# Optimization experiments

Hardware: AMD Instinct MI355X
Metric: run time of the kernel (lower is better)

Reference implementation:

```python
import jax, jax.numpy as jnp
import numpy as np

EPS = 1e-5  # BatchNorm2d default eps


def _bn_params(c, gamma):
    # rows: gamma, beta, running_mean, running_var (inference-mode BN)
    return jnp.stack([jnp.full((c,), gamma, jnp.float32),
                      jnp.zeros((c,), jnp.float32),
                      jnp.zeros((c,), jnp.float32),
                      jnp.ones((c,), jnp.float32)])


def _bn(x, p):
    g, b, m, v = p
    scale = (g / jnp.sqrt(v + EPS)).reshape(1, -1, 1, 1)
    return (x - m.reshape(1, -1, 1, 1)) * scale + b.reshape(1, -1, 1, 1)


def _conv1x1(x, w, b):
    # w: [O, C]; 1x1 Conv2d == channel matmul
    return jnp.einsum('oc,nctv->notv', w, x) + b[None, :, None, None]


def setup_inputs() -> dict:
    key = jax.random.key(0)
    N, C, COUT, T, V, S = 8, 64, 128, 256, 256, 3
    IC = COUT // 4  # coff_embedding = 4
    ks = jax.random.split(key, 10)
    rn = lambda k, shp, s=0.05: jax.random.normal(k, shp, jnp.float32) * s
    x = jax.random.normal(ks[0], (N, C, T, V), jnp.float32)
    mat_adj = jax.random.uniform(ks[1], (S, T, T), jnp.float32) * (1.0 / T)  # static adjacency
    adj_weight = jnp.full((S, T, T), 1e-6, jnp.float32)  # nn.init.constant_(weight, 1e-6)
    return {
        'x': x,
        'mat_adj': mat_adj,
        'adj_weight': adj_weight,
        'wa': rn(ks[2], (S, IC, C)), 'ba': jnp.zeros((S, IC), jnp.float32),
        'wb': rn(ks[3], (S, IC, C)), 'bb': jnp.zeros((S, IC), jnp.float32),
        'wd': rn(ks[4], (S, COUT, C)), 'bd': jnp.zeros((S, COUT), jnp.float32),
        'gcn_bn': _bn_params(COUT, 1e-6),  # util.init_bn(self.bn, 1e-6)
        'cres_w': rn(ks[5], (COUT, C)), 'cres_b': jnp.zeros((COUT,), jnp.float32),
        'cres_bn': _bn_params(COUT, 1.0),
        'tcn_w': rn(ks[6], (COUT, COUT, 9)), 'tcn_b': jnp.zeros((COUT,), jnp.float32),
        'tcn_bn': _bn_params(COUT, 1.0),
        'rt_w': rn(ks[7], (COUT, C)), 'rt_b': jnp.zeros((COUT,), jnp.float32),
        'rt_bn': _bn_params(COUT, 1.0),
    }


def reference(x, mat_adj, adj_weight, wa, ba, wb, bb, wd, bd, gcn_bn,
              cres_w, cres_b, cres_bn, tcn_w, tcn_b, tcn_bn, rt_w, rt_b, rt_bn):
    N, C, T, V = x.shape
    A = mat_adj + adj_weight  # [S, T, T]
    y = 0.0
    for i in range(A.shape[0]):  # num_subset = 3, structurally distinct weights
        a = _conv1x1(x, wa[i], ba[i])      # [N, IC, T, V]
        be = _conv1x1(x, wb[i], bb[i])     # [N, IC, T, V]
        # embed1 [N,T,IC*V] @ embed2 [N,IC*V,T] -> contract over (IC, V)
        scores = jnp.einsum('nctv,ncsv->nts', a, be) / V
        att = jax.nn.softmax(scores, axis=-2)  # Softmax(dim=-2)
        adapt = A[i] + att                      # [N, T, T]
        # mat_inpt [N,C*V,T] @ adapt -> view(N,C,V,T)
        xa = jnp.einsum('nctv,nts->ncvs', x, adapt)  # [N, C, V, T]
        y = y + _conv1x1(xa, wd[i], bd[i])           # [N, COUT, V, T]
    gcn = jax.nn.relu(_bn(y, gcn_bn) + _bn(_conv1x1(x, cres_w, cres_b), cres_bn))
    # UnitTSCN: Conv2d kernel (9,1), stride (1,1), padding (4,0), then BN
    t = jax.lax.conv_general_dilated(gcn, tcn_w[..., None], (1, 1), ((4, 4), (0, 0)),
                                     dimension_numbers=('NCHW', 'OIHW', 'NCHW'))
    t = _bn(t + tcn_b[None, :, None, None], tcn_bn)
    # residual path: UnitTSCN(kernel_size=1, stride=1) since in != out
    r = _bn(_conv1x1(x, rt_w, rt_b), rt_bn)
    return jax.nn.relu(t + r)
```

## Files before the change

kernel.cpp:

```cpp
#include <hip/hip_runtime.h>

typedef unsigned short u16;

#define DEVI static __device__ __forceinline__

DEVI float bf2f(u16 v) { return __uint_as_float(((unsigned)v) << 16); }
DEVI u16 f2bf(float f) {
  unsigned u = __float_as_uint(f);
  u += 0x7FFFu + ((u >> 16) & 1u);
  return (u16)(u >> 16);
}
DEVI float4 ld4bf(const u16* p) {
  ushort4 q = *(const ushort4*)p;
  return make_float4(bf2f(q.x), bf2f(q.y), bf2f(q.z), bf2f(q.w));
}

typedef __attribute__((ext_vector_type(8))) short short8;
typedef __attribute__((ext_vector_type(4))) float floatx4;


__global__ void k_diag(float* out, float v) { out[0] = v; }

__global__ __launch_bounds__(256) void k_ab2(
    const float* __restrict__ x, const float* __restrict__ wa, const float* __restrict__ ba,
    const float* __restrict__ wb, const float* __restrict__ bb,
    u16* __restrict__ a_buf, u16* __restrict__ b_buf, int sub)
{
  __shared__ __align__(16) u16 Aw[64 * 64];
  __shared__ __align__(16) u16 Bx[256 * 64];
  __shared__ float sbias[64];
  const int n = blockIdx.y;
  const int q0 = blockIdx.x << 8;
  const int tid = threadIdx.x;

  if (tid < 64) {
    sbias[tid] = (tid < 32) ? ba[sub * 32 + tid] : bb[sub * 32 + tid - 32];
  }
  {
    const int kq = tid & 15;
    const int rr = tid >> 4;
    #pragma unroll
    for (int j = 0; j < 4; ++j) {
      int r = rr + (j << 4);
      float4 wv = (r < 32) ? *(const float4*)(wa + sub * 2048 + r * 64 + kq * 4)
                           : *(const float4*)(wb + sub * 2048 + (r - 32) * 64 + kq * 4);
      int e = (r << 6) + (((kq >> 1) ^ (r & 7)) << 3) + ((kq & 1) << 2);
      *(ushort4*)&Aw[e] = make_ushort4(f2bf(wv.x), f2bf(wv.y), f2bf(wv.z), f2bf(wv.w));
    }
  }
  {
    const int q4 = (tid & 63) << 2;
    const int kb = (tid >> 6) << 4;
    u16 va[16][4];
    #pragma unroll
    for (int dk = 0; dk < 16; ++dk) {
      float4 f = *(const float4*)(x + (((size_t)(n << 6) + kb + dk) << 16) + q0 + q4);
      va[dk][0] = f2bf(f.x); va[dk][1] = f2bf(f.y);
      va[dk][2] = f2bf(f.z); va[dk][3] = f2bf(f.w);
    }
    const int g0 = kb >> 3;
    #pragma unroll
    for (int dq = 0; dq < 4; ++dq) {
      int q = q4 + dq;
      int e0 = (q << 6) + ((g0 ^ (q & 7)) << 3);
      *(ushort4*)&Bx[e0]     = make_ushort4(va[0][dq], va[1][dq], va[2][dq], va[3][dq]);
      *(ushort4*)&Bx[e0 + 4] = make_ushort4(va[4][dq], va[5][dq], va[6][dq], va[7][dq]);
      int e1 = (q << 6) + (((g0 + 1) ^ (q & 7)) << 3);
      *(ushort4*)&Bx[e1]     = make_ushort4(va[8][dq], va[9][dq], va[10][dq], va[11][dq]);
      *(ushort4*)&Bx[e1 + 4] = make_ushort4(va[12][dq], va[13][dq], va[14][dq], va[15][dq]);
    }
  }
  __syncthreads();

  const int lane = tid & 63, wave = tid >> 6;
  const int qw = wave << 6;
  const int l15 = lane & 15, lg = lane >> 4;
  floatx4 acc[4][4];
  #pragma unroll
  for (int m = 0; m < 4; ++m)
    #pragma unroll
    for (int nn = 0; nn < 4; ++nn) acc[m][nn] = (floatx4){0.f, 0.f, 0.f, 0.f};

  #pragma unroll
  for (int ks = 0; ks < 2; ++ks) {
    const int gk = (ks << 2) + lg;
    short8 av[4], bv[4];
    #pragma unroll
    for (int m = 0; m < 4; ++m) {
      int r = (m << 4) + l15;
      av[m] = *(const short8*)&Aw[(r << 6) + ((gk ^ (r & 7)) << 3)];
    }
    #pragma unroll
    for (int nn = 0; nn < 4; ++nn) {
      int q = qw + (nn << 4) + l15;
      bv[nn] = *(const short8*)&Bx[(q << 6) + ((gk ^ (q & 7)) << 3)];
    }
    #pragma unroll
    for (int m = 0; m < 4; ++m)
      #pragma unroll
      for (int nn = 0; nn < 4; ++nn)
        acc[m][nn] = __builtin_amdgcn_mfma_f32_16x16x32_bf16(av[m], bv[nn], acc[m][nn], 0, 0, 0);
  }

  #pragma unroll
  for (int m = 0; m < 4; ++m) {
    #pragma unroll
    for (int r = 0; r < 4; ++r) {
      int row = (m << 4) + (lg << 2) + r;
      float bias = sbias[row];
      u16* dst = (row < 32) ? a_buf + (((n * 32 + row) << 16) + q0)
                            : b_buf + (((n * 32 + row - 32) << 16) + q0);
      #pragma unroll
      for (int nn = 0; nn < 4; ++nn) {
        int q = qw + (nn << 4) + l15;
        dst[q] = f2bf(acc[m][nn][r] + bias);
      }
    }
  }
}

__global__ __launch_bounds__(256) void k_sc2(
    const u16* __restrict__ a_buf, const u16* __restrict__ b_buf,
    float* __restrict__ part)
{
  __shared__ __align__(16) u16 At[128 * 64];
  __shared__ __align__(16) u16 Bt[128 * 64];
  const int n = blockIdx.z;
  const int kg = blockIdx.y;
  const int t0 = (blockIdx.x >> 1) << 7;
  const int s0 = (blockIdx.x & 1) << 7;
  const int tid = threadIdx.x;
  const int lane = tid & 63, wave = tid >> 6;
  const int tw = (wave & 1) << 6;
  const int sw = (wave >> 1) << 6;
  const int l15 = lane & 15, lg = lane >> 4;
  const int g = tid & 7;
  const int trow = tid >> 3;

  floatx4 acc[4][4];
  #pragma unroll
  for (int m = 0; m < 4; ++m)
    #pragma unroll
    for (int nn = 0; nn < 4; ++nn) acc[m][nn] = (floatx4){0.f, 0.f, 0.f, 0.f};

  for (int cc = 0; cc < 4; ++cc) {
    const int c = (kg << 2) + cc;
    const u16* ap = a_buf + ((n * 32 + c) << 16);
    const u16* bp = b_buf + ((n * 32 + c) << 16);
    for (int vt = 0; vt < 4; ++vt) {
      const int v0 = vt << 6;
      __syncthreads();
      #pragma unroll
      for (int j = 0; j < 4; ++j) {
        int t = trow + (j << 5);
        int e = (t << 6) + ((g ^ (t & 7)) << 3);
        *(short8*)&At[e] = *(const short8*)(ap + (t0 + t) * 256 + v0 + g * 8);
        *(short8*)&Bt[e] = *(const short8*)(bp + (s0 + t) * 256 + v0 + g * 8);
      }
      __syncthreads();
      #pragma unroll
      for (int ks = 0; ks < 2; ++ks) {
        const int gk = (ks << 2) + lg;
        short8 av[4], bv[4];
        #pragma unroll
        for (int m = 0; m < 4; ++m) {
          int t = tw + (m << 4) + l15;
          av[m] = *(const short8*)&At[(t << 6) + ((gk ^ (t & 7)) << 3)];
        }
        #pragma unroll
        for (int nn = 0; nn < 4; ++nn) {
          int s = sw + (nn << 4) + l15;
          bv[nn] = *(const short8*)&Bt[(s << 6) + ((gk ^ (s & 7)) << 3)];
        }
        #pragma unroll
        for (int m = 0; m < 4; ++m)
          #pragma unroll
          for (int nn = 0; nn < 4; ++nn)
            acc[m][nn] = __builtin_amdgcn_mfma_f32_16x16x32_bf16(av[m], bv[nn], acc[m][nn], 0, 0, 0);
      }
    }
  }

  const float inv256 = 1.0f / 256.0f;
  float* pp = part + (((kg << 3) + n) << 16);
  #pragma unroll
  for (int m = 0; m < 4; ++m) {
    #pragma unroll
    for (int r = 0; r < 4; ++r) {
      int t = t0 + tw + (m << 4) + (lg << 2) + r;
      #pragma unroll
      for (int nn = 0; nn < 4; ++nn) {
        int s = s0 + sw + (nn << 4) + l15;
        pp[t * 256 + s] = acc[m][nn][r] * inv256;
      }
    }
  }
}

__global__ __launch_bounds__(256) void k_soft2(
    const float* __restrict__ part, const float* __restrict__ madj,
    const float* __restrict__ wadj, float* __restrict__ adapt, int sub)
{
  __shared__ float Ls[256][32];
  __shared__ float redm[8][32];
  __shared__ float reds[8][32];
  const int sc = blockIdx.x;
  const int n = blockIdx.y;
  const int tid = threadIdx.x;
  const int sl = tid & 31, tg = tid >> 5;
  const int s = (sc << 5) + sl;

  float m = -1e30f;
  for (int i = 0; i < 32; ++i) {
    int t = (tg << 5) + i;
    int off = t * 256 + s;
    float v = 0.f;
    #pragma unroll
    for (int k = 0; k < 8; ++k) v += part[(((k << 3) + n) << 16) + off];
    Ls[t][sl] = v;
    m = fmaxf(m, v);
  }
  redm[tg][sl] = m;
  __syncthreads();
  #pragma unroll
  for (int k = 0; k < 8; ++k) m = fmaxf(m, redm[k][sl]);
  float sum = 0.f;
  for (int i = 0; i < 32; ++i) {
    int t = (tg << 5) + i;
    sum += __expf(Ls[t][sl] - m);
  }
  reds[tg][sl] = sum;
  __syncthreads();
  float tot = 0.f;
  #pragma unroll
  for (int k = 0; k < 8; ++k) tot += reds[k][sl];
  float inv = 1.0f / tot;
  const float* ma = madj + (sub << 16);
  const float* wa2 = wadj + (sub << 16);
  float* adp = adapt + (n << 16);
  for (int i = 0; i < 32; ++i) {
    int t = (tg << 5) + i;
    int off = t * 256 + s;
    adp[off] = __expf(Ls[t][sl] - m) * inv + ma[off] + wa2[off];
  }
}

__global__ __launch_bounds__(256) void k_xa2(
    const float* __restrict__ x, const float* __restrict__ adapt,
    u16* __restrict__ xa)
{
  __shared__ __align__(16) u16 Av[128 * 64];
  __shared__ __align__(16) u16 Bs2[128 * 64];
  const int n = blockIdx.z, c = blockIdx.y;
  const int v0 = (blockIdx.x >> 1) << 7;
  const int s0 = (blockIdx.x & 1) << 7;
  const int tid = threadIdx.x;
  const int lane = tid & 63, wave = tid >> 6;
  const int vw = (wave & 1) << 6;
  const int sw = (wave >> 1) << 6;
  const int l15 = lane & 15, lg = lane >> 4;
  const int q4 = (tid & 31) << 2;
  const int kb = (tid >> 5) << 3;
  const float* xp = x + (((size_t)(n << 6) + c) << 16);
  const float* ap = adapt + (n << 16);

  floatx4 acc[4][4];
  #pragma unroll
  for (int m = 0; m < 4; ++m)
    #pragma unroll
    for (int nn = 0; nn < 4; ++nn) acc[m][nn] = (floatx4){0.f, 0.f, 0.f, 0.f};

  for (int kt = 0; kt < 4; ++kt) {
    const int tb = kt << 6;
    __syncthreads();
    {
      u16 va[8][4], vb[8][4];
      #pragma unroll
      for (int dk = 0; dk < 8; ++dk) {
        int t = tb + kb + dk;
        float4 fa = *(const float4*)(xp + (t << 8) + v0 + q4);
        float4 fb = *(const float4*)(ap + (t << 8) + s0 + q4);
        va[dk][0] = f2bf(fa.x); va[dk][1] = f2bf(fa.y);
        va[dk][2] = f2bf(fa.z); va[dk][3] = f2bf(fa.w);
        vb[dk][0] = f2bf(fb.x); vb[dk][1] = f2bf(fb.y);
        vb[dk][2] = f2bf(fb.z); vb[dk][3] = f2bf(fb.w);
      }
      const int g = kb >> 3;
      #pragma unroll
      for (int dq = 0; dq < 4; ++dq) {
        int q = q4 + dq;
        int e = (q << 6) + ((g ^ (q & 7)) << 3);
        *(ushort4*)&Av[e]      = make_ushort4(va[0][dq], va[1][dq], va[2][dq], va[3][dq]);
        *(ushort4*)&Av[e + 4]  = make_ushort4(va[4][dq], va[5][dq], va[6][dq], va[7][dq]);
        *(ushort4*)&Bs2[e]     = make_ushort4(vb[0][dq], vb[1][dq], vb[2][dq], vb[3][dq]);
        *(ushort4*)&Bs2[e + 4] = make_ushort4(vb[4][dq], vb[5][dq], vb[6][dq], vb[7][dq]);
      }
    }
    __syncthreads();
    #pragma unroll
    for (int ks = 0; ks < 2; ++ks) {
      const int gk = (ks << 2) + lg;
      short8 av[4], bv[4];
      #pragma unroll
      for (int m = 0; m < 4; ++m) {
        int v = vw + (m << 4) + l15;
        av[m] = *(const short8*)&Av[(v << 6) + ((gk ^ (v & 7)) << 3)];
      }
      #pragma unroll
      for (int nn = 0; nn < 4; ++nn) {
        int s = sw + (nn << 4) + l15;
        bv[nn] = *(const short8*)&Bs2[(s << 6) + ((gk ^ (s & 7)) << 3)];
      }
      #pragma unroll
      for (int m = 0; m < 4; ++m)
        #pragma unroll
        for (int nn = 0; nn < 4; ++nn)
          acc[m][nn] = __builtin_amdgcn_mfma_f32_16x16x32_bf16(av[m], bv[nn], acc[m][nn], 0, 0, 0);
    }
  }

  u16* xo = xa + (((n << 6) + c) << 16);
  #pragma unroll
  for (int m = 0; m < 4; ++m) {
    #pragma unroll
    for (int r = 0; r < 4; ++r) {
      int v = v0 + vw + (m << 4) + (lg << 2) + r;
      #pragma unroll
      for (int nn = 0; nn < 4; ++nn) {
        int s = s0 + sw + (nn << 4) + l15;
        xo[v * 256 + s] = f2bf(acc[m][nn][r]);
      }
    }
  }
}

__global__ __launch_bounds__(256) void k_gcnf(
    const u16* __restrict__ xa_all, const float* __restrict__ x,
    const float* __restrict__ wd, const float* __restrict__ bd,
    const float* __restrict__ cw, const float* __restrict__ cb,
    const float* __restrict__ cbn, const float* __restrict__ gbn,
    u16* __restrict__ gcn)
{
  __shared__ __align__(16) u16 Wt[128 * 64];
  __shared__ __align__(16) u16 Gt[128 * 64];
  __shared__ float s_kk[128], s_sg[128], s_sc[128];
  const int n = blockIdx.y;
  const int q0 = blockIdx.x << 7;
  const int tid = threadIdx.x;
  if (tid < 128) {
    int o = tid;
    float sg = gbn[o] * rsqrtf(gbn[384 + o] + 1e-5f);
    float sc = cbn[o] * rsqrtf(cbn[384 + o] + 1e-5f);
    s_sg[o] = sg; s_sc[o] = sc;
    s_kk[o] = sg * (bd[o] + bd[128 + o] + bd[256 + o])
            + (cb[o] - cbn[256 + o]) * sc + cbn[128 + o]
            - gbn[256 + o] * sg + gbn[128 + o];
  }
  __syncthreads();

  const int lane = tid & 63, wave = tid >> 6;
  const int ow = (wave & 1) << 6;
  const int qw = (wave >> 1) << 6;
  const int l15 = lane & 15, lg = lane >> 4;
  const int kq = tid & 15;
  const int orow = tid >> 4;
  const int q4 = (tid & 31) << 2;
  const int kb = (tid >> 5) << 3;

  floatx4 acc[4][4];
  #pragma unroll
  for (int m = 0; m < 4; ++m)
    #pragma unroll
    for (int nn = 0; nn < 4; ++nn) acc[m][nn] = (floatx4){0.f, 0.f, 0.f, 0.f};

  for (int kt = 0; kt < 6; ++kt) {
    __syncthreads();
    #pragma unroll
    for (int j = 0; j < 8; ++j) {
      int o = orow + (j << 4);
      int e = (o << 6) + (((kq >> 1) ^ (o & 7)) << 3) + ((kq & 1) << 2);
      if (kt < 3) {
        float4 wv = *(const float4*)(wd + kt * 8192 + o * 64 + kq * 4);
        float s = s_sg[o];
        *(ushort4*)&Wt[e] = make_ushort4(f2bf(s * wv.x), f2bf(s * wv.y),
                                         f2bf(s * wv.z), f2bf(s * wv.w));
      } else {
        float4 wv = *(const float4*)(cw + o * 64 + kq * 4);
        float s = s_sc[o];
        float f0 = s * wv.x, f1 = s * wv.y, f2 = s * wv.z, f3 = s * wv.w;
        u16 h0 = f2bf(f0), h1 = f2bf(f1), h2 = f2bf(f2), h3 = f2bf(f3);
        if (kt == 4)
          *(ushort4*)&Wt[e] = make_ushort4(f2bf(f0 - bf2f(h0)), f2bf(f1 - bf2f(h1)),
                                           f2bf(f2 - bf2f(h2)), f2bf(f3 - bf2f(h3)));
        else
          *(ushort4*)&Wt[e] = make_ushort4(h0, h1, h2, h3);
      }
    }
    {
      u16 va[8][4];
      if (kt < 3) {
        const u16* xp = xa_all + (size_t)kt * 33554432u + (((size_t)(n << 6) + kb) << 16);
        #pragma unroll
        for (int dk = 0; dk < 8; ++dk) {
          ushort4 t4 = *(const ushort4*)(xp + ((size_t)dk << 16) + q0 + q4);
          va[dk][0] = t4.x; va[dk][1] = t4.y; va[dk][2] = t4.z; va[dk][3] = t4.w;
        }
      } else {
        #pragma unroll
        for (int dk = 0; dk < 8; ++dk) {
          float4 f = *(const float4*)(x + (((size_t)(n << 6) + kb + dk) << 16) + q0 + q4);
          if (kt == 5) {
            u16 h0 = f2bf(f.x), h1 = f2bf(f.y), h2 = f2bf(f.z), h3 = f2bf(f.w);
            va[dk][0] = f2bf(f.x - bf2f(h0)); va[dk][1] = f2bf(f.y - bf2f(h1));
            va[dk][2] = f2bf(f.z - bf2f(h2)); va[dk][3] = f2bf(f.w - bf2f(h3));
          } else {
            va[dk][0] = f2bf(f.x); va[dk][1] = f2bf(f.y);
            va[dk][2] = f2bf(f.z); va[dk][3] = f2bf(f.w);
          }
        }
      }
      const int g = kb >> 3;
      #pragma unroll
      for (int dq = 0; dq < 4; ++dq) {
        int q = q4 + dq;
        int e = (q << 6) + ((g ^ (q & 7)) << 3);
        *(ushort4*)&Gt[e]     = make_ushort4(va[0][dq], va[1][dq], va[2][dq], va[3][dq]);
        *(ushort4*)&Gt[e + 4] = make_ushort4(va[4][dq], va[5][dq], va[6][dq], va[7][dq]);
      }
    }
    __syncthreads();
    #pragma unroll
    for (int ks = 0; ks < 2; ++ks) {
      const int gk = (ks << 2) + lg;
      short8 av[4], bv[4];
      #pragma unroll
      for (int m = 0; m < 4; ++m) {
        int o = ow + (m << 4) + l15;
        av[m] = *(const short8*)&Wt[(o << 6) + ((gk ^ (o & 7)) << 3)];
      }
      #pragma unroll
      for (int nn = 0; nn < 4; ++nn) {
        int q = qw + (nn << 4) + l15;
        bv[nn] = *(const short8*)&Gt[(q << 6) + ((gk ^ (q & 7)) << 3)];
      }
      #pragma unroll
      for (int m = 0; m < 4; ++m)
        #pragma unroll
        for (int nn = 0; nn < 4; ++nn)
          acc[m][nn] = __builtin_amdgcn_mfma_f32_16x16x32_bf16(av[m], bv[nn], acc[m][nn], 0, 0, 0);
    }
  }

  #pragma unroll
  for (int m = 0; m < 4; ++m) {
    #pragma unroll
    for (int r = 0; r < 4; ++r) {
      int o = ow + (m << 4) + (lg << 2) + r;
      float kadd = s_kk[o];
      u16* dst = gcn + (((n << 7) + o) << 16) + q0;
      #pragma unroll
      for (int nn = 0; nn < 4; ++nn) {
        int q = qw + (nn << 4) + l15;
        dst[q] = f2bf(fmaxf(acc[m][nn][r] + kadd, 0.f));
      }
    }
  }
}

__global__ __launch_bounds__(256) void k_out(
    const u16* __restrict__ gcn, const float* __restrict__ x,
    const float* __restrict__ tw, const float* __restrict__ tb, const float* __restrict__ tbn,
    const float* __restrict__ rw, const float* __restrict__ rb, const float* __restrict__ rbn,
    float* __restrict__ out)
{
  __shared__ __align__(16) u16 Wh[128 * 64];
  __shared__ __align__(16) u16 Wl[128 * 64];
  __shared__ __align__(16) u16 Gc[128 * 64];
  __shared__ float s_st[128], s_sr[128], s_kk[128];
  const int n = blockIdx.y;
  const int q0 = blockIdx.x << 7;
  const int h = q0 >> 8;
  const int w0 = q0 & 255;
  const int tid = threadIdx.x;
  if (tid < 128) {
    int o = tid;
    float st = tbn[o] * rsqrtf(tbn[384 + o] + 1e-5f);
    float sr = rbn[o] * rsqrtf(rbn[384 + o] + 1e-5f);
    s_st[o] = st; s_sr[o] = sr;
    s_kk[o] = (tb[o] - tbn[256 + o]) * st + tbn[128 + o]
            + (rb[o] - rbn[256 + o]) * sr + rbn[128 + o];
  }
  __syncthreads();

  const int lane = tid & 63;
  const int wave = tid >> 6;
  const int ow = (wave & 1) << 6;
  const int qw = (wave >> 1) << 6;
  const int l15 = lane & 15;
  const int lg  = lane >> 4;

  const int kq   = tid & 15;
  const int orow = tid >> 4;
  const int q4   = (tid & 31) << 2;
  const int kb   = (tid >> 5) << 3;

  floatx4 acc[4][4];
  #pragma unroll
  for (int m = 0; m < 4; ++m)
    #pragma unroll
    for (int nn = 0; nn < 4; ++nn)
      acc[m][nn] = (floatx4){0.f, 0.f, 0.f, 0.f};

  for (int kc = 0; kc < 19; ++kc) {
    __syncthreads();
    {
      const int k4 = (kc << 6) + (kq << 2);
      #pragma unroll
      for (int j = 0; j < 8; ++j) {
        int o = orow + (j << 4);
        float4 wv;
        float s;
        if (kc < 18) { wv = *(const float4*)(tw + o * 1152 + k4); s = s_st[o]; }
        else         { wv = *(const float4*)(rw + (o << 6) + (k4 - 1152)); s = s_sr[o]; }
        float f0 = s * wv.x, f1 = s * wv.y, f2 = s * wv.z, f3 = s * wv.w;
        u16 b0 = f2bf(f0), b1 = f2bf(f1), b2 = f2bf(f2), b3 = f2bf(f3);
        int e = (o << 6) + (((kq >> 1) ^ (o & 7)) << 3) + ((kq & 1) << 2);
        *(ushort4*)&Wh[e] = make_ushort4(b0, b1, b2, b3);
        *(ushort4*)&Wl[e] = make_ushort4(f2bf(f0 - bf2f(b0)), f2bf(f1 - bf2f(b1)),
                                         f2bf(f2 - bf2f(b2)), f2bf(f3 - bf2f(b3)));
      }
    }
    {
      u16 va[8][4];
      if (kc < 18) {
        #pragma unroll
        for (int dk = 0; dk < 8; ++dk) {
          int k = (kc << 6) + kb + dk;
          unsigned i = (unsigned)k / 9u;
          int kh = k - 9 * (int)i;
          int h2 = h + kh - 4;
          ushort4 t4;
          if ((unsigned)h2 < 256u)
            t4 = *(const ushort4*)(gcn + ((((n << 7) + (int)i) << 16) + (h2 << 8) + w0 + q4));
          else t4 = make_ushort4(0, 0, 0, 0);
          va[dk][0] = t4.x; va[dk][1] = t4.y; va[dk][2] = t4.z; va[dk][3] = t4.w;
        }
      } else {
        #pragma unroll
        for (int dk = 0; dk < 8; ++dk) {
          int c = kb + dk;
          float4 f = *(const float4*)(x + (((size_t)(n << 6) + c) << 16) + q0 + q4);
          va[dk][0] = f2bf(f.x); va[dk][1] = f2bf(f.y);
          va[dk][2] = f2bf(f.z); va[dk][3] = f2bf(f.w);
        }
      }
      #pragma unroll
      for (int dq = 0; dq < 4; ++dq) {
        int q = q4 + dq;
        int e = (q << 6) + ((((kb >> 3) ^ (q & 7))) << 3);
        *(ushort4*)&Gc[e]     = make_ushort4(va[0][dq], va[1][dq], va[2][dq], va[3][dq]);
        *(ushort4*)&Gc[e + 4] = make_ushort4(va[4][dq], va[5][dq], va[6][dq], va[7][dq]);
      }
    }
    __syncthreads();
    #pragma unroll
    for (int ks = 0; ks < 2; ++ks) {
      const int gk = (ks << 2) + lg;
      short8 ah[4], al[4], bg[4];
      #pragma unroll
      for (int m = 0; m < 4; ++m) {
        int o = ow + (m << 4) + l15;
        int e = (o << 6) + ((gk ^ (o & 7)) << 3);
        ah[m] = *(const short8*)&Wh[e];
        al[m] = *(const short8*)&Wl[e];
      }
      #pragma unroll
      for (int nn = 0; nn < 4; ++nn) {
        int q = qw + (nn << 4) + l15;
        int e = (q << 6) + ((gk ^ (q & 7)) << 3);
        bg[nn] = *(const short8*)&Gc[e];
      }
      #pragma unroll
      for (int m = 0; m < 4; ++m)
        #pragma unroll
        for (int nn = 0; nn < 4; ++nn) {
          acc[m][nn] = __builtin_amdgcn_mfma_f32_16x16x32_bf16(ah[m], bg[nn], acc[m][nn], 0, 0, 0);
          acc[m][nn] = __builtin_amdgcn_mfma_f32_16x16x32_bf16(al[m], bg[nn], acc[m][nn], 0, 0, 0);
        }
    }
  }

  #pragma unroll
  for (int m = 0; m < 4; ++m) {
    #pragma unroll
    for (int r = 0; r < 4; ++r) {
      int o = ow + (m << 4) + (lg << 2) + r;
      float kadd = s_kk[o];
      float* dst = out + (((size_t)((n << 7) + o)) << 16) + q0;
      #pragma unroll
      for (int nn = 0; nn < 4; ++nn) {
        int q = qw + (nn << 4) + l15;
        dst[q] = fmaxf(acc[m][nn][r] + kadd, 0.f);
      }
    }
  }
}

extern "C" void kernel_launch(void* const* d_in, const int* in_sizes, int n_in,
                              void* d_out, int out_size, void* d_ws, size_t ws_size,
                              hipStream_t stream) {
  const float* x       = (const float*)d_in[0];
  const float* mat_adj = (const float*)d_in[1];
  const float* adj_w   = (const float*)d_in[2];
  const float* wa      = (const float*)d_in[3];
  const float* ba      = (const float*)d_in[4];
  const float* wb      = (const float*)d_in[5];
  const float* bb      = (const float*)d_in[6];
  const float* wd      = (const float*)d_in[7];
  const float* bd      = (const float*)d_in[8];
  const float* gcn_bn  = (const float*)d_in[9];
  const float* cres_w  = (const float*)d_in[10];
  const float* cres_b  = (const float*)d_in[11];
  const float* cres_bn = (const float*)d_in[12];
  const float* tcn_w   = (const float*)d_in[13];
  const float* tcn_b   = (const float*)d_in[14];
  const float* tcn_bn  = (const float*)d_in[15];
  const float* rt_w    = (const float*)d_in[16];
  const float* rt_b    = (const float*)d_in[17];
  const float* rt_bn   = (const float*)d_in[18];
  float* out = (float*)d_out;

  (void)hipGetLastError();

  hipMemsetAsync(d_out, 0x42, 4, stream);

  if (n_in != 19)                    { k_diag<<<1,1,0,stream>>>(out, 2019.f); return; }
  if (in_sizes[0]  != 33554432)      { k_diag<<<1,1,0,stream>>>(out, 2000.f); return; }
  if (in_sizes[3]  != 6144)          { k_diag<<<1,1,0,stream>>>(out, 2003.f); return; }
  if (in_sizes[7]  != 24576)         { k_diag<<<1,1,0,stream>>>(out, 2007.f); return; }
  if (in_sizes[9]  != 512)           { k_diag<<<1,1,0,stream>>>(out, 2009.f); return; }
  if (in_sizes[13] != 147456)        { k_diag<<<1,1,0,stream>>>(out, 2013.f); return; }
  if (in_sizes[16] != 8192)          { k_diag<<<1,1,0,stream>>>(out, 2016.f); return; }
  if (out_size != 67108864)          { k_diag<<<1,1,0,stream>>>(out, 3000.f); return; }
  if (ws_size < 134217728ull)        { k_diag<<<1,1,0,stream>>>(out, (float)ws_size); return; }

  float* wsf   = (float*)d_ws;
  u16*   a_buf = (u16*)d_ws;
  u16*   b_buf = a_buf + 16777216;
  float* part  = wsf + 16777216;
  float* adapt = wsf + 20971520;
  u16*   gcn   = (u16*)d_ws;
  u16*   xa_all = (u16*)d_out;

  for (int i = 0; i < 3; ++i) {
    k_ab2  <<<dim3(256, 8),   256, 0, stream>>>(x, wa, ba, wb, bb, a_buf, b_buf, i);
    k_sc2  <<<dim3(4, 8, 8),  256, 0, stream>>>(a_buf, b_buf, part);
    k_soft2<<<dim3(8, 8),     256, 0, stream>>>(part, mat_adj, adj_w, adapt, i);
    k_xa2  <<<dim3(4, 64, 8), 256, 0, stream>>>(x, adapt, xa_all + (size_t)i * 33554432u);
  }
  k_gcnf<<<dim3(512, 8), 256, 0, stream>>>(xa_all, x, wd, bd, cres_w, cres_b,
                                           cres_bn, gcn_bn, gcn);
  k_out<<<dim3(512, 8), 256, 0, stream>>>(gcn, x, tcn_w, tcn_b, tcn_bn,
                                          rt_w, rt_b, rt_bn, out);

  hipError_t le = hipGetLastError();
  if (le != hipSuccess) {
    k_diag<<<1, 1, 0, stream>>>(out, 1.0e9f + (float)(int)le);
  }
}
```

Baseline: 1.502 ms.

## Pre-transpose x to bf16 once, use packed bf16 converts and new LDS swizzle

Adds a k_xt kernel that converts x to bf16 and transposes it to [N,C,V,T] once. The three k_xa2 launches then load their A operand as direct 16-byte bf16 copies instead of reconverting fp32 x with scattered 4-element LDS stores each time. Every fp32->bf16 conversion now uses the packed v_cvt_pk_bf16_f32 instruction. LDS staging stores are widened to 16-byte writes with a two-level XOR swizzle, and per-lane LDS offsets are precomputed outside the k-loops. The cost is an extra launch and an extra bf16 copy of x stored in the spare tail of the output buffer.

```diff
diff --git a/kernel.cpp b/kernel.cpp
--- a/kernel.cpp
+++ b/kernel.cpp
@@ -10,16 +10,56 @@
   u += 0x7FFFu + ((u >> 16) & 1u);
   return (u16)(u >> 16);
 }
-DEVI float4 ld4bf(const u16* p) {
-  ushort4 q = *(const ushort4*)p;
-  return make_float4(bf2f(q.x), bf2f(q.y), bf2f(q.z), bf2f(q.w));
+DEVI unsigned pk2bf(float a, float b) {
+  unsigned r;
+  asm("v_cvt_pk_bf16_f32 %0, %1, %2" : "=v"(r) : "v"(a), "v"(b));
+  return r;
 }
 
 typedef __attribute__((ext_vector_type(8))) short short8;
 typedef __attribute__((ext_vector_type(4))) float floatx4;
 
+#define GSWZ(q, g) (((q) << 6) + ((((g) ^ ((q) & 7) ^ (((q) >> 3) & 7))) << 3))
+
 
 __global__ void k_diag(float* out, float v) { out[0] = v; }
+
+__global__ __launch_bounds__(256) void k_xt(
+    const float* __restrict__ x, u16* __restrict__ xt)
+{
+  __shared__ __align__(16) u16 Ls[256 * 64];
+  const int n = blockIdx.z, c = blockIdx.y, t0 = blockIdx.x << 6;
+  const int tid = threadIdx.x;
+  const float* xp = x + (((size_t)(n << 6) + c) << 16);
+  const int t4 = (tid & 15) << 2;
+  #pragma unroll
+  for (int j = 0; j < 4; ++j) {
+    const int v4 = ((tid >> 4) << 2) + (j << 6);
+    float4 f0 = *(const float4*)(xp + ((t0 + t4 + 0) << 8) + v4);
+    float4 f1 = *(const float4*)(xp + ((t0 + t4 + 1) << 8) + v4);
+    float4 f2 = *(const float4*)(xp + ((t0 + t4 + 2) << 8) + v4);
+    float4 f3 = *(const float4*)(xp + ((t0 + t4 + 3) << 8) + v4);
+    const float fr[4][4] = {{f0.x,f1.x,f2.x,f3.x},{f0.y,f1.y,f2.y,f3.y},
+                            {f0.z,f1.z,f2.z,f3.z},{f0.w,f1.w,f2.w,f3.w}};
+    #pragma unroll
+    for (int dv = 0; dv < 4; ++dv) {
+      int v = v4 + dv;
+      unsigned p0 = pk2bf(fr[dv][0], fr[dv][1]);
+      unsigned p1 = pk2bf(fr[dv][2], fr[dv][3]);
+      int e = (v << 6) + (((t4 >> 3) ^ (v & 7)) << 3) + (t4 & 4);
+      *(uint2*)&Ls[e] = make_uint2(p0, p1);
+    }
+  }
+  __syncthreads();
+  const int g = tid & 7;
+  u16* xo = xt + (((size_t)((n << 6) + c)) << 16) + t0;
+  #pragma unroll
+  for (int it = 0; it < 8; ++it) {
+    int v = (tid >> 3) + (it << 5);
+    short8 row = *(const short8*)&Ls[(v << 6) + ((g ^ (v & 7)) << 3)];
+    *(short8*)(xo + (v << 8) + (g << 3)) = row;
+  }
+}
 
 __global__ __launch_bounds__(256) void k_ab2(
     const float* __restrict__ x, const float* __restrict__ wa, const float* __restrict__ ba,
@@ -33,41 +73,37 @@
   const int q0 = blockIdx.x << 8;
   const int tid = threadIdx.x;
 
-  if (tid < 64) {
-    sbias[tid] = (tid < 32) ? ba[sub * 32 + tid] : bb[sub * 32 + tid - 32];
-  }
+  if (tid < 64) sbias[tid] = (tid < 32) ? ba[sub * 32 + tid] : bb[sub * 32 + tid - 32];
   {
     const int kq = tid & 15;
     const int rr = tid >> 4;
     #pragma unroll
     for (int j = 0; j < 4; ++j) {
       int r = rr + (j << 4);
-      float4 wv = (r < 32) ? *(const float4*)(wa + sub * 2048 + r * 64 + kq * 4)
-                           : *(const float4*)(wb + sub * 2048 + (r - 32) * 64 + kq * 4);
+      float4 wv = (r < 32) ? *(const float4*)(wa + sub * 2048 + r * 64 + (kq << 2))
+                           : *(const float4*)(wb + sub * 2048 + (r - 32) * 64 + (kq << 2));
       int e = (r << 6) + (((kq >> 1) ^ (r & 7)) << 3) + ((kq & 1) << 2);
-      *(ushort4*)&Aw[e] = make_ushort4(f2bf(wv.x), f2bf(wv.y), f2bf(wv.z), f2bf(wv.w));
+      *(uint2*)&Aw[e] = make_uint2(pk2bf(wv.x, wv.y), pk2bf(wv.z, wv.w));
     }
   }
   {
     const int q4 = (tid & 63) << 2;
     const int kb = (tid >> 6) << 4;
-    u16 va[16][4];
-    #pragma unroll
-    for (int dk = 0; dk < 16; ++dk) {
-      float4 f = *(const float4*)(x + (((size_t)(n << 6) + kb + dk) << 16) + q0 + q4);
-      va[dk][0] = f2bf(f.x); va[dk][1] = f2bf(f.y);
-      va[dk][2] = f2bf(f.z); va[dk][3] = f2bf(f.w);
-    }
-    const int g0 = kb >> 3;
-    #pragma unroll
-    for (int dq = 0; dq < 4; ++dq) {
-      int q = q4 + dq;
-      int e0 = (q << 6) + ((g0 ^ (q & 7)) << 3);
-      *(ushort4*)&Bx[e0]     = make_ushort4(va[0][dq], va[1][dq], va[2][dq], va[3][dq]);
-      *(ushort4*)&Bx[e0 + 4] = make_ushort4(va[4][dq], va[5][dq], va[6][dq], va[7][dq]);
-      int e1 = (q << 6) + (((g0 + 1) ^ (q & 7)) << 3);
-      *(ushort4*)&Bx[e1]     = make_ushort4(va[8][dq], va[9][dq], va[10][dq], va[11][dq]);
-      *(ushort4*)&Bx[e1 + 4] = make_ushort4(va[12][dq], va[13][dq], va[14][dq], va[15][dq]);
+    #pragma unroll
+    for (int half = 0; half < 2; ++half) {
+      float fa[8][4];
+      #pragma unroll
+      for (int dk = 0; dk < 8; ++dk)
+        *(float4*)fa[dk] = *(const float4*)(x + (((size_t)(n << 6) + kb + half * 8 + dk) << 16) + q0 + q4);
+      const int G = (kb >> 3) + half;
+      #pragma unroll
+      for (int dq = 0; dq < 4; ++dq) {
+        unsigned w0 = pk2bf(fa[0][dq], fa[1][dq]);
+        unsigned w1 = pk2bf(fa[2][dq], fa[3][dq]);
+        unsigned w2 = pk2bf(fa[4][dq], fa[5][dq]);
+        unsigned w3 = pk2bf(fa[6][dq], fa[7][dq]);
+        *(uint4*)&Bx[GSWZ(q4 + dq, G)] = make_uint4(w0, w1, w2, w3);
+      }
     }
   }
   __syncthreads();
@@ -75,6 +111,12 @@
   const int lane = tid & 63, wave = tid >> 6;
   const int qw = wave << 6;
   const int l15 = lane & 15, lg = lane >> 4;
+  int aoff[4], boff[4];
+  #pragma unroll
+  for (int m = 0; m < 4; ++m) { int r = (m << 4) + l15; aoff[m] = (r << 6) + ((r & 7) << 3); }
+  #pragma unroll
+  for (int nn = 0; nn < 4; ++nn) { int q = qw + (nn << 4) + l15; boff[nn] = GSWZ(q, 0); }
+
   floatx4 acc[4][4];
   #pragma unroll
   for (int m = 0; m < 4; ++m)
@@ -83,18 +125,12 @@
 
   #pragma unroll
   for (int ks = 0; ks < 2; ++ks) {
-    const int gk = (ks << 2) + lg;
+    const int gs = ((ks << 2) + lg) << 3;
     short8 av[4], bv[4];
     #pragma unroll
-    for (int m = 0; m < 4; ++m) {
-      int r = (m << 4) + l15;
-      av[m] = *(const short8*)&Aw[(r << 6) + ((gk ^ (r & 7)) << 3)];
-    }
-    #pragma unroll
-    for (int nn = 0; nn < 4; ++nn) {
-      int q = qw + (nn << 4) + l15;
-      bv[nn] = *(const short8*)&Bx[(q << 6) + ((gk ^ (q & 7)) << 3)];
-    }
+    for (int m = 0; m < 4; ++m) av[m] = *(const short8*)&Aw[aoff[m] ^ gs];
+    #pragma unroll
+    for (int nn = 0; nn < 4; ++nn) bv[nn] = *(const short8*)&Bx[boff[nn] ^ gs];
     #pragma unroll
     for (int m = 0; m < 4; ++m)
       #pragma unroll
@@ -111,9 +147,10 @@
       u16* dst = (row < 32) ? a_buf + (((n * 32 + row) << 16) + q0)
                             : b_buf + (((n * 32 + row - 32) << 16) + q0);
       #pragma unroll
-      for (int nn = 0; nn < 4; ++nn) {
-        int q = qw + (nn << 4) + l15;
-        dst[q] = f2bf(acc[m][nn][r] + bias);
+      for (int np = 0; np < 2; ++np) {
+        unsigned p = pk2bf(acc[m][2 * np][r] + bias, acc[m][2 * np + 1][r] + bias);
+        dst[qw + np * 32 + l15] = (u16)p;
+        dst[qw + np * 32 + 16 + l15] = (u16)(p >> 16);
       }
     }
   }
@@ -137,6 +174,12 @@
   const int g = tid & 7;
   const int trow = tid >> 3;
 
+  int aoff[4], boff[4];
+  #pragma unroll
+  for (int m = 0; m < 4; ++m) { int t = tw + (m << 4) + l15; aoff[m] = (t << 6) + ((t & 7) << 3); }
+  #pragma unroll
+  for (int nn = 0; nn < 4; ++nn) { int s = sw + (nn << 4) + l15; boff[nn] = (s << 6) + ((s & 7) << 3); }
+
   floatx4 acc[4][4];
   #pragma unroll
   for (int m = 0; m < 4; ++m)
@@ -160,18 +203,12 @@
       __syncthreads();
       #pragma unroll
       for (int ks = 0; ks < 2; ++ks) {
-        const int gk = (ks << 2) + lg;
+        const int gs = ((ks << 2) + lg) << 3;
         short8 av[4], bv[4];
         #pragma unroll
-        for (int m = 0; m < 4; ++m) {
-          int t = tw + (m << 4) + l15;
-          av[m] = *(const short8*)&At[(t << 6) + ((gk ^ (t & 7)) << 3)];
-        }
-        #pragma unroll
-        for (int nn = 0; nn < 4; ++nn) {
-          int s = sw + (nn << 4) + l15;
-          bv[nn] = *(const short8*)&Bt[(s << 6) + ((gk ^ (s & 7)) << 3)];
-        }
+        for (int m = 0; m < 4; ++m) av[m] = *(const short8*)&At[aoff[m] ^ gs];
+        #pragma unroll
+        for (int nn = 0; nn < 4; ++nn) bv[nn] = *(const short8*)&Bt[boff[nn] ^ gs];
         #pragma unroll
         for (int m = 0; m < 4; ++m)
           #pragma unroll
@@ -246,23 +283,28 @@
 }
 
 __global__ __launch_bounds__(256) void k_xa2(
-    const float* __restrict__ x, const float* __restrict__ adapt,
+    const u16* __restrict__ xt, const float* __restrict__ adapt,
     u16* __restrict__ xa)
 {
   __shared__ __align__(16) u16 Av[128 * 64];
-  __shared__ __align__(16) u16 Bs2[128 * 64];
+  __shared__ __align__(16) u16 Bt2[128 * 64];
   const int n = blockIdx.z, c = blockIdx.y;
   const int v0 = (blockIdx.x >> 1) << 7;
   const int s0 = (blockIdx.x & 1) << 7;
   const int tid = threadIdx.x;
   const int lane = tid & 63, wave = tid >> 6;
-  const int vw = (wave & 1) << 6;
-  const int sw = (wave >> 1) << 6;
+  const int vw = (wave & 1) << 6, sw = (wave >> 1) << 6;
   const int l15 = lane & 15, lg = lane >> 4;
-  const int q4 = (tid & 31) << 2;
-  const int kb = (tid >> 5) << 3;
-  const float* xp = x + (((size_t)(n << 6) + c) << 16);
+  const int ga = tid & 7, vr = tid >> 3;
+  const int q4 = (tid & 31) << 2, kb = (tid >> 5) << 3;
+  const u16* xp = xt + (((size_t)((n << 6) + c)) << 16);
   const float* ap = adapt + (n << 16);
+
+  int aoff[4], boff[4];
+  #pragma unroll
+  for (int m = 0; m < 4; ++m) { int v = vw + (m << 4) + l15; aoff[m] = (v << 6) + ((v & 7) << 3); }
+  #pragma unroll
+  for (int nn = 0; nn < 4; ++nn) { int s = sw + (nn << 4) + l15; boff[nn] = GSWZ(s, 0); }
 
   floatx4 acc[4][4];
   #pragma unroll
@@ -273,44 +315,36 @@
   for (int kt = 0; kt < 4; ++kt) {
     const int tb = kt << 6;
     __syncthreads();
+    #pragma unroll
+    for (int j = 0; j < 4; ++j) {
+      int v = vr + (j << 5);
+      *(short8*)&Av[(v << 6) + ((ga ^ (v & 7)) << 3)] =
+        *(const short8*)(xp + ((v0 + v) << 8) + tb + (ga << 3));
+    }
     {
-      u16 va[8][4], vb[8][4];
-      #pragma unroll
-      for (int dk = 0; dk < 8; ++dk) {
-        int t = tb + kb + dk;
-        float4 fa = *(const float4*)(xp + (t << 8) + v0 + q4);
-        float4 fb = *(const float4*)(ap + (t << 8) + s0 + q4);
-        va[dk][0] = f2bf(fa.x); va[dk][1] = f2bf(fa.y);
-        va[dk][2] = f2bf(fa.z); va[dk][3] = f2bf(fa.w);
-        vb[dk][0] = f2bf(fb.x); vb[dk][1] = f2bf(fb.y);
-        vb[dk][2] = f2bf(fb.z); vb[dk][3] = f2bf(fb.w);
-      }
-      const int g = kb >> 3;
+      float fa[8][4];
+      #pragma unroll
+      for (int dk = 0; dk < 8; ++dk)
+        *(float4*)fa[dk] = *(const float4*)(ap + ((tb + kb + dk) << 8) + s0 + q4);
+      const int G = kb >> 3;
       #pragma unroll
       for (int dq = 0; dq < 4; ++dq) {
-        int q = q4 + dq;
-        int e = (q << 6) + ((g ^ (q & 7)) << 3);
-        *(ushort4*)&Av[e]      = make_ushort4(va[0][dq], va[1][dq], va[2][dq], va[3][dq]);
-        *(ushort4*)&Av[e + 4]  = make_ushort4(va[4][dq], va[5][dq], va[6][dq], va[7][dq]);
-        *(ushort4*)&Bs2[e]     = make_ushort4(vb[0][dq], vb[1][dq], vb[2][dq], vb[3][dq]);
-        *(ushort4*)&Bs2[e + 4] = make_ushort4(vb[4][dq], vb[5][dq], vb[6][dq], vb[7][dq]);
+        unsigned w0 = pk2bf(fa[0][dq], fa[1][dq]);
+        unsigned w1 = pk2bf(fa[2][dq], fa[3][dq]);
+        unsigned w2 = pk2bf(fa[4][dq], fa[5][dq]);
+        unsigned w3 = pk2bf(fa[6][dq], fa[7][dq]);
+        *(uint4*)&Bt2[GSWZ(q4 + dq, G)] = make_uint4(w0, w1, w2, w3);
       }
     }
     __syncthreads();
     #pragma unroll
     for (int ks = 0; ks < 2; ++ks) {
-      const int gk = (ks << 2) + lg;
+      const int gs = ((ks << 2) + lg) << 3;
       short8 av[4], bv[4];
       #pragma unroll
-      for (int m = 0; m < 4; ++m) {
-        int v = vw + (m << 4) + l15;
-        av[m] = *(const short8*)&Av[(v << 6) + ((gk ^ (v & 7)) << 3)];
-      }
-      #pragma unroll
-      for (int nn = 0; nn < 4; ++nn) {
-        int s = sw + (nn << 4) + l15;
-        bv[nn] = *(const short8*)&Bs2[(s << 6) + ((gk ^ (s & 7)) << 3)];
-      }
+      for (int m = 0; m < 4; ++m) av[m] = *(const short8*)&Av[aoff[m] ^ gs];
+      #pragma unroll
+      for (int nn = 0; nn < 4; ++nn) bv[nn] = *(const short8*)&Bt2[boff[nn] ^ gs];
       #pragma unroll
       for (int m = 0; m < 4; ++m)
         #pragma unroll
@@ -325,10 +359,12 @@
     #pragma unroll
     for (int r = 0; r < 4; ++r) {
       int v = v0 + vw + (m << 4) + (lg << 2) + r;
-      #pragma unroll
-      for (int nn = 0; nn < 4; ++nn) {
-        int s = s0 + sw + (nn << 4) + l15;
-        xo[v * 256 + s] = f2bf(acc[m][nn][r]);
+      u16* dst = xo + v * 256 + s0;
+      #pragma unroll
+      for (int np = 0; np < 2; ++np) {
+        unsigned p = pk2bf(acc[m][2 * np][r], acc[m][2 * np + 1][r]);
+        dst[sw + np * 32 + l15] = (u16)p;
+        dst[sw + np * 32 + 16 + l15] = (u16)(p >> 16);
       }
     }
   }
@@ -367,6 +403,12 @@
   const int q4 = (tid & 31) << 2;
   const int kb = (tid >> 5) << 3;
 
+  int aoff[4], boff[4];
+  #pragma unroll
+  for (int m = 0; m < 4; ++m) { int o = ow + (m << 4) + l15; aoff[m] = (o << 6) + ((o & 7) << 3); }
+  #pragma unroll
+  for (int nn = 0; nn < 4; ++nn) { int q = qw + (nn << 4) + l15; boff[nn] = GSWZ(q, 0); }
+
   floatx4 acc[4][4];
   #pragma unroll
   for (int m = 0; m < 4; ++m)
@@ -380,69 +422,71 @@
       int o = orow + (j << 4);
       int e = (o << 6) + (((kq >> 1) ^ (o & 7)) << 3) + ((kq & 1) << 2);
       if (kt < 3) {
-        float4 wv = *(const float4*)(wd + kt * 8192 + o * 64 + kq * 4);
+        float4 wv = *(const float4*)(wd + kt * 8192 + o * 64 + (kq << 2));
         float s = s_sg[o];
-        *(ushort4*)&Wt[e] = make_ushort4(f2bf(s * wv.x), f2bf(s * wv.y),
-                                         f2bf(s * wv.z), f2bf(s * wv.w));
+        *(uint2*)&Wt[e] = make_uint2(pk2bf(s * wv.x, s * wv.y), pk2bf(s * wv.z, s * wv.w));
       } else {
-        float4 wv = *(const float4*)(cw + o * 64 + kq * 4);
+        float4 wv = *(const float4*)(cw + o * 64 + (kq << 2));
         float s = s_sc[o];
         float f0 = s * wv.x, f1 = s * wv.y, f2 = s * wv.z, f3 = s * wv.w;
-        u16 h0 = f2bf(f0), h1 = f2bf(f1), h2 = f2bf(f2), h3 = f2bf(f3);
-        if (kt == 4)
-          *(ushort4*)&Wt[e] = make_ushort4(f2bf(f0 - bf2f(h0)), f2bf(f1 - bf2f(h1)),
-                                           f2bf(f2 - bf2f(h2)), f2bf(f3 - bf2f(h3)));
-        else
-          *(ushort4*)&Wt[e] = make_ushort4(h0, h1, h2, h3);
-      }
-    }
-    {
-      u16 va[8][4];
+        unsigned h01 = pk2bf(f0, f1), h23 = pk2bf(f2, f3);
+        if (kt == 4) {
+          float g0 = __uint_as_float(h01 << 16), g1 = __uint_as_float(h01 & 0xffff0000u);
+          float g2 = __uint_as_float(h23 << 16), g3 = __uint_as_float(h23 & 0xffff0000u);
+          *(uint2*)&Wt[e] = make_uint2(pk2bf(f0 - g0, f1 - g1), pk2bf(f2 - g2, f3 - g3));
+        } else {
+          *(uint2*)&Wt[e] = make_uint2(h01, h23);
+        }
+      }
+    }
+    if (kt != 4) {
+      const int G = kb >> 3;
       if (kt < 3) {
         const u16* xp = xa_all + (size_t)kt * 33554432u + (((size_t)(n << 6) + kb) << 16);
+        u16 va[8][4];
         #pragma unroll
         for (int dk = 0; dk < 8; ++dk) {
           ushort4 t4 = *(const ushort4*)(xp + ((size_t)dk << 16) + q0 + q4);
           va[dk][0] = t4.x; va[dk][1] = t4.y; va[dk][2] = t4.z; va[dk][3] = t4.w;
         }
+        #pragma unroll
+        for (int dq = 0; dq < 4; ++dq) {
+          unsigned p0 = (unsigned)va[0][dq] | ((unsigned)va[1][dq] << 16);
+          unsigned p1 = (unsigned)va[2][dq] | ((unsigned)va[3][dq] << 16);
+          unsigned p2 = (unsigned)va[4][dq] | ((unsigned)va[5][dq] << 16);
+          unsigned p3 = (unsigned)va[6][dq] | ((unsigned)va[7][dq] << 16);
+          *(uint4*)&Gt[GSWZ(q4 + dq, G)] = make_uint4(p0, p1, p2, p3);
+        }
       } else {
-        #pragma unroll
-        for (int dk = 0; dk < 8; ++dk) {
-          float4 f = *(const float4*)(x + (((size_t)(n << 6) + kb + dk) << 16) + q0 + q4);
-          if (kt == 5) {
-            u16 h0 = f2bf(f.x), h1 = f2bf(f.y), h2 = f2bf(f.z), h3 = f2bf(f.w);
-            va[dk][0] = f2bf(f.x - bf2f(h0)); va[dk][1] = f2bf(f.y - bf2f(h1));
-            va[dk][2] = f2bf(f.z - bf2f(h2)); va[dk][3] = f2bf(f.w - bf2f(h3));
-          } else {
-            va[dk][0] = f2bf(f.x); va[dk][1] = f2bf(f.y);
-            va[dk][2] = f2bf(f.z); va[dk][3] = f2bf(f.w);
+        float fa[8][4];
+        #pragma unroll
+        for (int dk = 0; dk < 8; ++dk)
+          *(float4*)fa[dk] = *(const float4*)(x + (((size_t)(n << 6) + kb + dk) << 16) + q0 + q4);
+        #pragma unroll
+        for (int dq = 0; dq < 4; ++dq) {
+          unsigned p[4];
+          #pragma unroll
+          for (int k2 = 0; k2 < 4; ++k2) {
+            unsigned h = pk2bf(fa[2 * k2][dq], fa[2 * k2 + 1][dq]);
+            if (kt == 5) {
+              float g0 = __uint_as_float(h << 16), g1 = __uint_as_float(h & 0xffff0000u);
+              h = pk2bf(fa[2 * k2][dq] - g0, fa[2 * k2 + 1][dq] - g1);
+            }
+            p[k2] = h;
           }
+          *(uint4*)&Gt[GSWZ(q4 + dq, G)] = make_uint4(p[0], p[1], p[2], p[3]);
         }
       }
-      const int g = kb >> 3;
-      #pragma unroll
-      for (int dq = 0; dq < 4; ++dq) {
-        int q = q4 + dq;
-        int e = (q << 6) + ((g ^ (q & 7)) << 3);
-        *(ushort4*)&Gt[e]     = make_ushort4(va[0][dq], va[1][dq], va[2][dq], va[3][dq]);
-        *(ushort4*)&Gt[e + 4] = make_ushort4(va[4][dq], va[5][dq], va[6][dq], va[7][dq]);
-      }
     }
     __syncthreads();
     #pragma unroll
     for (int ks = 0; ks < 2; ++ks) {
-      const int gk = (ks << 2) + lg;
+      const int gs = ((ks << 2) + lg) << 3;
       short8 av[4], bv[4];
       #pragma unroll
-      for (int m = 0; m < 4; ++m) {
-        int o = ow + (m << 4) + l15;
-        av[m] = *(const short8*)&Wt[(o << 6) + ((gk ^ (o & 7)) << 3)];
-      }
-      #pragma unroll
-      for (int nn = 0; nn < 4; ++nn) {
-        int q = qw + (nn << 4) + l15;
-        bv[nn] = *(const short8*)&Gt[(q << 6) + ((gk ^ (q & 7)) << 3)];
-      }
+      for (int m = 0; m < 4; ++m) av[m] = *(const short8*)&Wt[aoff[m] ^ gs];
+      #pragma unroll
+      for (int nn = 0; nn < 4; ++nn) bv[nn] = *(const short8*)&Gt[boff[nn] ^ gs];
       #pragma unroll
       for (int m = 0; m < 4; ++m)
         #pragma unroll
@@ -459,9 +503,12 @@
       float kadd = s_kk[o];
       u16* dst = gcn + (((n << 7) + o) << 16) + q0;
       #pragma unroll
-      for (int nn = 0; nn < 4; ++nn) {
-        int q = qw + (nn << 4) + l15;
-        dst[q] = f2bf(fmaxf(acc[m][nn][r] + kadd, 0.f));
+      for (int np = 0; np < 2; ++np) {
+        float v0 = fmaxf(acc[m][2 * np][r] + kadd, 0.f);
+        float v1 = fmaxf(acc[m][2 * np + 1][r] + kadd, 0.f);
+        unsigned p = pk2bf(v0, v1);
+        dst[qw + np * 32 + l15] = (u16)p;
+        dst[qw + np * 32 + 16 + l15] = (u16)(p >> 16);
       }
     }
   }
@@ -504,6 +551,16 @@
   const int q4   = (tid & 31) << 2;
   const int kb   = (tid >> 5) << 3;
 
+  float stj[8], srj[8];
+  #pragma unroll
+  for (int j = 0; j < 8; ++j) { int o = orow + (j << 4); stj[j] = s_st[o]; srj[j] = s_sr[o]; }
+
+  int aoff[4], boff[4];
+  #pragma unroll
+  for (int m = 0; m < 4; ++m) { int o = ow + (m << 4) + l15; aoff[m] = (o << 6) + ((o & 7) << 3); }
+  #pragma unroll
+  for (int nn = 0; nn < 4; ++nn) { int q = qw + (nn << 4) + l15; boff[nn] = GSWZ(q, 0); }
+
   floatx4 acc[4][4];
   #pragma unroll
   for (int m = 0; m < 4; ++m)
@@ -520,19 +577,22 @@
         int o = orow + (j << 4);
         float4 wv;
         float s;
-        if (kc < 18) { wv = *(const float4*)(tw + o * 1152 + k4); s = s_st[o]; }
-        else         { wv = *(const float4*)(rw + (o << 6) + (k4 - 1152)); s = s_sr[o]; }
+        if (kc < 18) { wv = *(const float4*)(tw + o * 1152 + k4); s = stj[j]; }
+        else         { wv = *(const float4*)(rw + (o << 6) + (k4 - 1152)); s = srj[j]; }
         float f0 = s * wv.x, f1 = s * wv.y, f2 = s * wv.z, f3 = s * wv.w;
-        u16 b0 = f2bf(f0), b1 = f2bf(f1), b2 = f2bf(f2), b3 = f2bf(f3);
+        unsigned h01 = pk2bf(f0, f1), h23 = pk2bf(f2, f3);
+        float g0 = __uint_as_float(h01 << 16), g1 = __uint_as_float(h01 & 0xffff0000u);
+        float g2 = __uint_as_float(h23 << 16), g3 = __uint_as_float(h23 & 0xffff0000u);
+        unsigned l01 = pk2bf(f0 - g0, f1 - g1), l23 = pk2bf(f2 - g2, f3 - g3);
         int e = (o << 6) + (((kq >> 1) ^ (o & 7)) << 3) + ((kq & 1) << 2);
-        *(ushort4*)&Wh[e] = make_ushort4(b0, b1, b2, b3);
-        *(ushort4*)&Wl[e] = make_ushort4(f2bf(f0 - bf2f(b0)), f2bf(f1 - bf2f(b1)),
-                                         f2bf(f2 - bf2f(b2)), f2bf(f3 - bf2f(b3)));
+        *(uint2*)&Wh[e] = make_uint2(h01, h23);
+        *(uint2*)&Wl[e] = make_uint2(l01, l23);
       }
     }
     {
-      u16 va[8][4];
+      const int G = kb >> 3;
       if (kc < 18) {
+        u16 va[8][4];
         #pragma unroll
         for (int dk = 0; dk < 8; ++dk) {
           int k = (kc << 6) + kb + dk;
@@ -545,41 +605,42 @@
           else t4 = make_ushort4(0, 0, 0, 0);
           va[dk][0] = t4.x; va[dk][1] = t4.y; va[dk][2] = t4.z; va[dk][3] = t4.w;
         }
+        #pragma unroll
+        for (int dq = 0; dq < 4; ++dq) {
+          unsigned p0 = (unsigned)va[0][dq] | ((unsigned)va[1][dq] << 16);
+          unsigned p1 = (unsigned)va[2][dq] | ((unsigned)va[3][dq] << 16);
+          unsigned p2 = (unsigned)va[4][dq] | ((unsigned)va[5][dq] << 16);
+          unsigned p3 = (unsigned)va[6][dq] | ((unsigned)va[7][dq] << 16);
+          *(uint4*)&Gc[GSWZ(q4 + dq, G)] = make_uint4(p0, p1, p2, p3);
+        }
       } else {
-        #pragma unroll
-        for (int dk = 0; dk < 8; ++dk) {
-          int c = kb + dk;
-          float4 f = *(const float4*)(x + (((size_t)(n << 6) + c) << 16) + q0 + q4);
-          va[dk][0] = f2bf(f.x); va[dk][1] = f2bf(f.y);
-          va[dk][2] = f2bf(f.z); va[dk][3] = f2bf(f.w);
+        float fa[8][4];
+        #pragma unroll
+        for (int dk = 0; dk < 8; ++dk)
+          *(float4*)fa[dk] = *(const float4*)(x + (((size_t)(n << 6) + kb + dk) << 16) + q0 + q4);
+        #pragma unroll
+        for (int dq = 0; dq < 4; ++dq) {
+          unsigned w0_ = pk2bf(fa[0][dq], fa[1][dq]);
+          unsigned w1_ = pk2bf(fa[2][dq], fa[3][dq]);
+          unsigned w2_ = pk2bf(fa[4][dq], fa[5][dq]);
+          unsigned w3_ = pk2bf(fa[6][dq], fa[7][dq]);
+          *(uint4*)&Gc[GSWZ(q4 + dq, G)] = make_uint4(w0_, w1_, w2_, w3_);
         }
       }
-      #pragma unroll
-      for (int dq = 0; dq < 4; ++dq) {
-        int q = q4 + dq;
-        int e = (q << 6) + ((((kb >> 3) ^ (q & 7))) << 3);
-        *(ushort4*)&Gc[e]     = make_ushort4(va[0][dq], va[1][dq], va[2][dq], va[3][dq]);
-        *(ushort4*)&Gc[e + 4] = make_ushort4(va[4][dq], va[5][dq], va[6][dq], va[7][dq]);
-      }
     }
     __syncthreads();
     #pragma unroll
     for (int ks = 0; ks < 2; ++ks) {
-      const int gk = (ks << 2) + lg;
+      const int gs = ((ks << 2) + lg) << 3;
       short8 ah[4], al[4], bg[4];
       #pragma unroll
       for (int m = 0; m < 4; ++m) {
-        int o = ow + (m << 4) + l15;
-        int e = (o << 6) + ((gk ^ (o & 7)) << 3);
-        ah[m] = *(const short8*)&Wh[e];
-        al[m] = *(const short8*)&Wl[e];
-      }
-      #pragma unroll
-      for (int nn = 0; nn < 4; ++nn) {
-        int q = qw + (nn << 4) + l15;
-        int e = (q << 6) + ((gk ^ (q & 7)) << 3);
-        bg[nn] = *(const short8*)&Gc[e];
-      }
+        ah[m] = *(const short8*)&Wh[aoff[m] ^ gs];
+        al[m] = *(const short8*)&Wl[aoff[m] ^ gs];
+      }
+      #pragma unroll
+      for (int nn = 0; nn < 4; ++nn)
+        bg[nn] = *(const short8*)&Gc[boff[nn] ^ gs];
       #pragma unroll
       for (int m = 0; m < 4; ++m)
         #pragma unroll
@@ -651,12 +712,14 @@
   float* adapt = wsf + 20971520;
   u16*   gcn   = (u16*)d_ws;
   u16*   xa_all = (u16*)d_out;
-
+  u16*   x_t   = ((u16*)d_out) + 100663296;
+
+  k_xt<<<dim3(4, 64, 8), 256, 0, stream>>>(x, x_t);
   for (int i = 0; i < 3; ++i) {
     k_ab2  <<<dim3(256, 8),   256, 0, stream>>>(x, wa, ba, wb, bb, a_buf, b_buf, i);
     k_sc2  <<<dim3(4, 8, 8),  256, 0, stream>>>(a_buf, b_buf, part);
     k_soft2<<<dim3(8, 8),     256, 0, stream>>>(part, mat_adj, adj_w, adapt, i);
-    k_xa2  <<<dim3(4, 64, 8), 256, 0, stream>>>(x, adapt, xa_all + (size_t)i * 33554432u);
+    k_xa2  <<<dim3(4, 64, 8), 256, 0, stream>>>(x_t, adapt, xa_all + (size_t)i * 33554432u);
   }
   k_gcnf<<<dim3(512, 8), 256, 0, stream>>>(xa_all, x, wd, bd, cres_w, cres_b,
                                            cres_bn, gcn_bn, gcn);
```

New measurement: 1.605 ms. 1.07x slower.
